# Kernel tuning notes

Measured on AMD Instinct MI355X. Metric: run time of the kernel, lower is better.

Reference implementation:

```python
import jax, jax.numpy as jnp
import numpy as np

SPATIAL_SHAPES = [(100, 100), (50, 50), (25, 25), (13, 13)]  # (h, w) per level
D_MODEL, N_HEADS, N_LEVELS, N_POINTS = 256, 8, 4, 4
B = 2
S = sum(h * w for h, w in SPATIAL_SHAPES)  # 13294
Q = S  # encoder self-attention: num_queries == sequence_length


def setup_inputs() -> dict:
    key = jax.random.key(0)
    ks = jax.random.split(key, 12)
    d = D_MODEL
    hlp = N_HEADS * N_LEVELS * N_POINTS
    scale = 0.02
    starts = np.cumsum([0] + [h * w for h, w in SPATIAL_SHAPES[:-1]])
    return {
        "hidden_states": jax.random.normal(ks[0], (B, Q, d), jnp.float32),
        "encoder_hidden_states": jax.random.normal(ks[1], (B, S, d), jnp.float32),
        "reference_points": jax.random.uniform(ks[2], (B, Q, N_LEVELS, 2), jnp.float32),
        "W_value": jax.random.normal(ks[3], (d, d), jnp.float32) * scale,
        "b_value": jnp.zeros((d,), jnp.float32),
        "W_off": jax.random.normal(ks[4], (d, hlp * 2), jnp.float32) * scale,
        "b_off": jax.random.normal(ks[5], (hlp * 2,), jnp.float32) * scale,
        "W_attn": jax.random.normal(ks[6], (d, hlp), jnp.float32) * scale,
        "b_attn": jnp.zeros((hlp,), jnp.float32),
        "W_out": jax.random.normal(ks[7], (d, d), jnp.float32) * scale,
        "b_out": jnp.zeros((d,), jnp.float32),
        "spatial_shapes": jnp.asarray(SPATIAL_SHAPES, jnp.int32),
        "level_start_index": jnp.asarray(starts, jnp.int32),
    }


def bilinear_sample(img, grid):
    # img: [N, C, h, w]; grid: [N, Q, P, 2] xy in [-1, 1]
    # F.grid_sample(mode='bilinear', padding_mode='zeros', align_corners=False)
    N, C, h, w = img.shape
    Qg, Pg = grid.shape[1], grid.shape[2]
    x = ((grid[..., 0] + 1.0) * w - 1.0) * 0.5
    y = ((grid[..., 1] + 1.0) * h - 1.0) * 0.5
    x0 = jnp.floor(x)
    y0 = jnp.floor(y)
    x1 = x0 + 1.0
    y1 = y0 + 1.0
    wx1 = x - x0
    wx0 = 1.0 - wx1
    wy1 = y - y0
    wy0 = 1.0 - wy1
    img_flat = img.reshape(N, C, h * w)

    def gather(xi, yi):
        valid = (xi >= 0) & (xi <= w - 1) & (yi >= 0) & (yi <= h - 1)
        xi_c = jnp.clip(xi, 0, w - 1).astype(jnp.int32)
        yi_c = jnp.clip(yi, 0, h - 1).astype(jnp.int32)
        idx = (yi_c * w + xi_c).reshape(N, 1, Qg * Pg)
        vals = jnp.take_along_axis(img_flat, idx, axis=2)  # [N, C, Q*P]
        return vals * valid.reshape(N, 1, Qg * Pg).astype(img.dtype)

    out = (
        gather(x0, y0) * (wx0 * wy0).reshape(N, 1, -1)
        + gather(x1, y0) * (wx1 * wy0).reshape(N, 1, -1)
        + gather(x0, y1) * (wx0 * wy1).reshape(N, 1, -1)
        + gather(x1, y1) * (wx1 * wy1).reshape(N, 1, -1)
    )
    return out.reshape(N, C, Qg, Pg)


def reference(hidden_states, encoder_hidden_states, reference_points,
              W_value, b_value, W_off, b_off, W_attn, b_attn, W_out, b_out,
              spatial_shapes, level_start_index):
    Bq, Qn, d = hidden_states.shape
    H, L, P = N_HEADS, N_LEVELS, N_POINTS
    Dh = d // H
    value = (encoder_hidden_states @ W_value + b_value).reshape(Bq, -1, H, Dh)
    off = (hidden_states @ W_off + b_off).reshape(Bq, Qn, H, L, P, 2)
    aw = (hidden_states @ W_attn + b_attn).reshape(Bq, Qn, H, L * P)
    aw = jax.nn.softmax(aw, axis=-1).reshape(Bq, Qn, H, L, P)
    # offset normalizer is (width, height) per level
    norm = jnp.stack([spatial_shapes[:, 1], spatial_shapes[:, 0]], -1).astype(off.dtype)
    loc = reference_points[:, :, None, :, None, :] + off / norm[None, None, None, :, None, :]
    grids = 2.0 * loc - 1.0  # [B, Q, H, L, P, 2]

    starts = np.cumsum([0] + [h * w for h, w in SPATIAL_SHAPES])
    sampled = []
    for lvl, (h, w) in enumerate(SPATIAL_SHAPES):
        v = value[:, starts[lvl]:starts[lvl + 1]]              # [B, h*w, H, Dh]
        v = v.transpose(0, 2, 3, 1).reshape(Bq * H, Dh, h, w)   # [B*H, Dh, h, w]
        g = grids[:, :, :, lvl].transpose(0, 2, 1, 3, 4).reshape(Bq * H, Qn, P, 2)
        sampled.append(bilinear_sample(v, g))                   # [B*H, Dh, Q, P]
    samp = jnp.stack(sampled, axis=-2).reshape(Bq * H, Dh, Qn, L * P)
    wts = aw.transpose(0, 2, 1, 3, 4).reshape(Bq * H, 1, Qn, L * P)
    out = (samp * wts).sum(-1)                                  # [B*H, Dh, Q]
    out = out.reshape(Bq, H * Dh, Qn).transpose(0, 2, 1)        # [B, Q, d]
    out = out @ W_out + b_out
    return out, aw
```

## Files before the change

kernel.cpp:

```cpp
#include <hip/hip_runtime.h>
#include <hip/hip_bf16.h>
#include <math.h>

#define BQn 2
#define QN 13294
#define SN 13294
#define NH 8
#define DH 32
#define DM 256

typedef __attribute__((ext_vector_type(8))) short short8;
typedef __attribute__((ext_vector_type(4))) float f32x4;

__device__ __forceinline__ unsigned short f2bf(float x) {
    union { float f; unsigned int u; } c; c.f = x;
    unsigned int r = c.u + 0x7fff + ((c.u >> 16) & 1);
    return (unsigned short)(r >> 16);
}
__device__ __forceinline__ float asf(unsigned int u) {
    union { unsigned int i; float f; } c; c.i = u; return c.f;
}

__global__ __launch_bounds__(256) void conv_weights(
    const float* __restrict__ Wv, const float* __restrict__ Woff,
    const float* __restrict__ Wa, const float* __restrict__ Wout,
    unsigned short* __restrict__ WvT, unsigned short* __restrict__ WoffT,
    unsigned short* __restrict__ WaT, unsigned short* __restrict__ WoutT)
{
    const int t = blockIdx.x * 256 + threadIdx.x;
    if (t < 65536) {
        const int n = t & 255, k = t >> 8;
        WvT[(size_t)n * 256 + k] = f2bf(Wv[(size_t)k * 256 + n]);
    } else if (t < 131072) {
        const int i = t - 65536, n = i & 255, k = i >> 8;
        WoffT[(size_t)n * 256 + k] = f2bf(Woff[(size_t)k * 256 + n]);
    } else if (t < 163840) {
        const int i = t - 131072, n = i & 127, k = i >> 7;
        WaT[(size_t)n * 256 + k] = f2bf(Wa[(size_t)k * 128 + n]);
    } else if (t < 229376) {
        const int i = t - 163840, n = i & 255, k = i >> 8;
        WoutT[(size_t)n * 256 + k] = f2bf(Wout[(size_t)k * 256 + n]);
    }
}

template<int N, int MODE, bool AF32>
__global__ __launch_bounds__(256) void gemm_mfma(
    const void* __restrict__ Av,
    const unsigned short* __restrict__ WT,
    const float* __restrict__ bias0,
    const float* __restrict__ bias1,
    void* __restrict__ Cv, int M)
{
    __shared__ unsigned short As[64][72];
    __shared__ unsigned short Bs[128][72];
    const int tid  = threadIdx.x;
    const int lane = tid & 63, wid = tid >> 6;
    const int wr = wid >> 1, wc = wid & 1;
    const int r0 = blockIdx.y * 64, n0 = blockIdx.x * 128;

    f32x4 acc[2][4] = {};

    for (int k0 = 0; k0 < 256; k0 += 64) {
        #pragma unroll
        for (int i = 0; i < 2; ++i) {
            const int idx = i * 256 + tid;
            const int row = idx >> 3, ch = (idx & 7) << 3;
            int grow = r0 + row; if (grow >= M) grow = M - 1;
            if (AF32) {
                const float* Af = (const float*)Av;
                const float4 v0 = *(const float4*)(Af + (size_t)grow * 256 + k0 + ch);
                const float4 v1 = *(const float4*)(Af + (size_t)grow * 256 + k0 + ch + 4);
                union { __hip_bfloat162 b[4]; uint4 u; } pk;
                pk.b[0] = __float22bfloat162_rn(make_float2(v0.x, v0.y));
                pk.b[1] = __float22bfloat162_rn(make_float2(v0.z, v0.w));
                pk.b[2] = __float22bfloat162_rn(make_float2(v1.x, v1.y));
                pk.b[3] = __float22bfloat162_rn(make_float2(v1.z, v1.w));
                *(uint4*)&As[row][ch] = pk.u;
            } else {
                const unsigned short* Ab = (const unsigned short*)Av;
                *(uint4*)&As[row][ch] =
                    *(const uint4*)(Ab + (size_t)grow * 256 + k0 + ch);
            }
        }
        #pragma unroll
        for (int i = 0; i < 4; ++i) {
            const int idx = i * 256 + tid;
            const int row = idx >> 3, ch = (idx & 7) << 3;
            *(uint4*)&Bs[row][ch] =
                *(const uint4*)(WT + (size_t)(n0 + row) * 256 + k0 + ch);
        }
        __syncthreads();
        #pragma unroll
        for (int kk = 0; kk < 2; ++kk) {
            const int kb = kk * 32 + (lane >> 4) * 8;
            short8 bfr[4];
            #pragma unroll
            for (int n = 0; n < 4; ++n)
                bfr[n] = *(const short8*)&Bs[wc * 64 + n * 16 + (lane & 15)][kb];
            #pragma unroll
            for (int m = 0; m < 2; ++m) {
                const short8 afr =
                    *(const short8*)&As[wr * 32 + m * 16 + (lane & 15)][kb];
                #pragma unroll
                for (int n = 0; n < 4; ++n)
                    acc[m][n] = __builtin_amdgcn_mfma_f32_16x16x32_bf16(
                        afr, bfr[n], acc[m][n], 0, 0, 0);
            }
        }
        __syncthreads();
    }

    #pragma unroll
    for (int m = 0; m < 2; ++m)
        #pragma unroll
        for (int n = 0; n < 4; ++n) {
            const int col = n0 + wc * 64 + n * 16 + (lane & 15);
            const float bsv = (col < 256) ? bias0[col] : bias1[col - 256];
            #pragma unroll
            for (int j = 0; j < 4; ++j) {
                const int row = r0 + wr * 32 + m * 16 + (lane >> 4) * 4 + j;
                if (row >= M) continue;
                const float v = acc[m][n][j] + bsv;
                if (MODE == 0) {
                    ((float*)Cv)[(size_t)row * N + col] = v;
                } else {
                    const int b = (row >= SN), s = row - b * SN;
                    const int h = col >> 5, dh = col & 31;
                    ((unsigned short*)Cv)
                        [(((size_t)b * NH + h) * SN + s) * DH + dh] = f2bf(v);
                }
            }
        }
}

__global__ __launch_bounds__(256) void ms_sample(
    const unsigned short* __restrict__ value,
    const float* __restrict__ offaw,
    const float* __restrict__ refp,
    unsigned short* __restrict__ outh,
    float* __restrict__ awout)
{
    const int h  = blockIdx.x & 7;
    const int qc = blockIdx.x >> 3;
    const int lc = threadIdx.x & 7;
    const int bq = qc * 32 + (threadIdx.x >> 3);
    if (bq >= BQn * QN) return;
    const int b  = (bq >= QN);
    const int gbase = threadIdx.x & 56;

    const float* rowp = offaw + (size_t)bq * 384;

    const float2 lw2 = *(const float2*)(rowp + 256 + h * 16 + lc * 2);
    float m = fmaxf(lw2.x, lw2.y);
    #pragma unroll
    for (int d = 1; d < 8; d <<= 1) m = fmaxf(m, __shfl_xor(m, d, 8));
    float e0 = __expf(lw2.x - m), e1 = __expf(lw2.y - m);
    float s = e0 + e1;
    #pragma unroll
    for (int d = 1; d < 8; d <<= 1) s += __shfl_xor(s, d, 8);
    const float inv = 1.f / s;
    e0 *= inv; e1 *= inv;
    *(float2*)(awout + (size_t)bq * 128 + h * 16 + lc * 2) = make_float2(e0, e1);

    const int lvl = lc >> 1;
    const int wi  = (lvl == 0) ? 100 : (lvl == 1) ? 50 : (lvl == 2) ? 25 : 13;
    const float fw = (float)wi;
    const int sti = (lvl == 0) ? 0 : (lvl == 1) ? 10000 : (lvl == 2) ? 12500 : 13125;
    const float rw = (lvl == 0) ? 0.01f : (lvl == 1) ? 0.02f
                   : (lvl == 2) ? 0.04f : (1.0f / 13.0f);
    const float2 rp = *(const float2*)(refp + (size_t)bq * 8 + lvl * 2);
    const float4 o4 = *(const float4*)(rowp + h * 32 + lc * 4);

    int   rA0, rB0, cA0, cB0, rA1, rB1, cA1, cB1;
    float wxA0, wxB0, wyA0, wyB0, wxA1, wxB1, wyA1, wyB1;

    auto prep = [&](float ox, float oy, float ek,
                    int& rA, int& rB, int& cA, int& cB,
                    float& wxA, float& wxB, float& wyA, float& wyB) {
        const float x = fmaf(fmaf(ox, rw, rp.x), fw, -0.5f);
        const float y = fmaf(fmaf(oy, rw, rp.y), fw, -0.5f);
        const float x0f = floorf(x), y0f = floorf(y);
        const int ix = (int)x0f, iy = (int)y0f;
        const float wx1 = x - x0f, wy1 = y - y0f;
        wxA = ((unsigned)ix        < (unsigned)wi) ? 1.f - wx1 : 0.f;
        wxB = ((unsigned)(ix + 1)  < (unsigned)wi) ? wx1       : 0.f;
        wyA = (((unsigned)iy       < (unsigned)wi) ? 1.f - wy1 : 0.f) * ek;
        wyB = (((unsigned)(iy + 1) < (unsigned)wi) ? wy1       : 0.f) * ek;
        const int xc0 = min(max(ix, 0),     wi - 1);
        const int xc1 = min(max(ix + 1, 0), wi - 1);
        const int yc0 = min(max(iy, 0),     wi - 1);
        const int yc1 = min(max(iy + 1, 0), wi - 1);
        rA = sti + yc0 * wi; rB = sti + yc1 * wi;
        cA = xc0;            cB = xc1;
    };
    prep(o4.x, o4.y, e0, rA0, rB0, cA0, cB0, wxA0, wxB0, wyA0, wyB0);
    prep(o4.z, o4.w, e1, rA1, rB1, cA1, cB1, wxA1, wxB1, wyA1, wyB1);

    const char* hplane = (const char*)(value + (size_t)h * SN * DH);
    const unsigned lnoff = (unsigned)b * (NH * SN * DH * 2) + lc * 8;

    float ax = 0.f, ay = 0.f, az = 0.f, aw_ = 0.f;

    #pragma unroll
    for (int p = 0; p < 16; ++p) {
        const int src = gbase + (p >> 1);
        const int   rA  = __shfl((p & 1) ? rA1  : rA0,  src, 64);
        const int   rB  = __shfl((p & 1) ? rB1  : rB0,  src, 64);
        const int   cA  = __shfl((p & 1) ? cA1  : cA0,  src, 64);
        const int   cB  = __shfl((p & 1) ? cB1  : cB0,  src, 64);
        const float wxA = __shfl((p & 1) ? wxA1 : wxA0, src, 64);
        const float wxB = __shfl((p & 1) ? wxB1 : wxB0, src, 64);
        const float wyA = __shfl((p & 1) ? wyA1 : wyA0, src, 64);
        const float wyB = __shfl((p & 1) ? wyB1 : wyB0, src, 64);

        #pragma unroll
        for (int c = 0; c < 4; ++c) {
            const int cell  = ((c >> 1) ? rB : rA) + ((c & 1) ? cB : cA);
            const float cw  = ((c & 1) ? wxB : wxA) * ((c >> 1) ? wyB : wyA);
            const uint2 v = *(const uint2*)(hplane + ((unsigned)cell * 64u + lnoff));
            ax  = fmaf(cw, asf(v.x << 16),          ax);
            ay  = fmaf(cw, asf(v.x & 0xffff0000u),  ay);
            az  = fmaf(cw, asf(v.y << 16),          az);
            aw_ = fmaf(cw, asf(v.y & 0xffff0000u),  aw_);
        }
    }

    ushort4 o;
    o.x = f2bf(ax); o.y = f2bf(ay); o.z = f2bf(az); o.w = f2bf(aw_);
    *(ushort4*)(outh + (size_t)bq * 256 + h * 32 + lc * 4) = o;
}

extern "C" void kernel_launch(void* const* d_in, const int* in_sizes, int n_in,
                              void* d_out, int out_size, void* d_ws, size_t ws_size,
                              hipStream_t stream) {
    const float* hs   = (const float*)d_in[0];
    const float* enc  = (const float*)d_in[1];
    const float* refp = (const float*)d_in[2];
    const float* Wv   = (const float*)d_in[3];
    const float* bv   = (const float*)d_in[4];
    const float* Woff = (const float*)d_in[5];
    const float* boff = (const float*)d_in[6];
    const float* Wa   = (const float*)d_in[7];
    const float* ba   = (const float*)d_in[8];
    const float* Wout = (const float*)d_in[9];
    const float* bout = (const float*)d_in[10];

    float* out    = (float*)d_out;
    float* aw_out = out + (size_t)BQn * QN * 256;

    const size_t MQ = (size_t)BQn * QN;
    unsigned short* valueb = (unsigned short*)d_ws;
    float* offaw = (float*)(valueb + MQ * 256);
    unsigned short* outh  = (unsigned short*)(offaw + MQ * 384);
    unsigned short* WvT   = outh + MQ * 256;
    unsigned short* WcatT = WvT + 256 * 256;
    unsigned short* WoutT = WcatT + 384 * 256;

    const int M = (int)MQ;
    const dim3 blk(256);

    conv_weights<<<896, blk, 0, stream>>>(Wv, Woff, Wa, Wout,
                                          WvT, WcatT, WcatT + 65536, WoutT);

    const int my = (M + 63) / 64;
    gemm_mfma<256, 1, true ><<<dim3(2, my), blk, 0, stream>>>(
        enc, WvT, bv, bv, valueb, M);
    gemm_mfma<384, 0, true ><<<dim3(3, my), blk, 0, stream>>>(
        hs, WcatT, boff, ba, offaw, M);

    const int qchunks = (M + 31) / 32;
    ms_sample<<<8 * qchunks, blk, 0, stream>>>(valueb, offaw, refp,
                                               outh, aw_out);

    gemm_mfma<256, 0, false><<<dim3(2, my), blk, 0, stream>>>(
        outh, WoutT, bout, bout, out, M);
}
```

Measured before the change: 130.2 us.

## Use 128-wide K tiles with register prefetch in the MFMA GEMM

The GEMM's K loop changes from four 64-wide tiles to two 128-wide tiles. Global loads for the second tile go into registers while MFMAs run on the first, which overlaps memory latency with compute and halves the number of barrier rounds. In exchange, shared memory roughly doubles and register pressure rises from the prefetch buffers, which may lower occupancy.

Result: slower. 181.8 us (+39.7%).

```diff
diff --git a/kernel.cpp b/kernel.cpp
--- a/kernel.cpp
+++ b/kernel.cpp
@@ -51,47 +51,70 @@
     const float* __restrict__ bias1,
     void* __restrict__ Cv, int M)
 {
-    __shared__ unsigned short As[64][72];
-    __shared__ unsigned short Bs[128][72];
+    __shared__ unsigned short As[64][136];
+    __shared__ unsigned short Bs[128][136];
     const int tid  = threadIdx.x;
     const int lane = tid & 63, wid = tid >> 6;
     const int wr = wid >> 1, wc = wid & 1;
     const int r0 = blockIdx.y * 64, n0 = blockIdx.x * 128;
 
-    f32x4 acc[2][4] = {};
-
-    for (int k0 = 0; k0 < 256; k0 += 64) {
-        #pragma unroll
-        for (int i = 0; i < 2; ++i) {
+    float4 paf[4][2];
+    uint4  pa[4];
+    uint4  pb[8];
+
+    auto LOADA = [&](int k0) {
+        #pragma unroll
+        for (int i = 0; i < 4; ++i) {
             const int idx = i * 256 + tid;
-            const int row = idx >> 3, ch = (idx & 7) << 3;
+            const int row = idx >> 4, ch = (idx & 15) << 3;
             int grow = r0 + row; if (grow >= M) grow = M - 1;
             if (AF32) {
                 const float* Af = (const float*)Av;
-                const float4 v0 = *(const float4*)(Af + (size_t)grow * 256 + k0 + ch);
-                const float4 v1 = *(const float4*)(Af + (size_t)grow * 256 + k0 + ch + 4);
+                paf[i][0] = *(const float4*)(Af + (size_t)grow * 256 + k0 + ch);
+                paf[i][1] = *(const float4*)(Af + (size_t)grow * 256 + k0 + ch + 4);
+            } else {
+                pa[i] = *(const uint4*)((const unsigned short*)Av
+                                        + (size_t)grow * 256 + k0 + ch);
+            }
+        }
+    };
+    auto LOADB = [&](int k0) {
+        #pragma unroll
+        for (int i = 0; i < 8; ++i) {
+            const int idx = i * 256 + tid;
+            const int row = idx >> 4, ch = (idx & 15) << 3;
+            pb[i] = *(const uint4*)(WT + (size_t)(n0 + row) * 256 + k0 + ch);
+        }
+    };
+    auto STORE = [&]() {
+        #pragma unroll
+        for (int i = 0; i < 4; ++i) {
+            const int idx = i * 256 + tid;
+            const int row = idx >> 4, ch = (idx & 15) << 3;
+            if (AF32) {
                 union { __hip_bfloat162 b[4]; uint4 u; } pk;
-                pk.b[0] = __float22bfloat162_rn(make_float2(v0.x, v0.y));
-                pk.b[1] = __float22bfloat162_rn(make_float2(v0.z, v0.w));
-                pk.b[2] = __float22bfloat162_rn(make_float2(v1.x, v1.y));
-                pk.b[3] = __float22bfloat162_rn(make_float2(v1.z, v1.w));
+                pk.b[0] = __float22bfloat162_rn(make_float2(paf[i][0].x, paf[i][0].y));
+                pk.b[1] = __float22bfloat162_rn(make_float2(paf[i][0].z, paf[i][0].w));
+                pk.b[2] = __float22bfloat162_rn(make_float2(paf[i][1].x, paf[i][1].y));
+                pk.b[3] = __float22bfloat162_rn(make_float2(paf[i][1].z, paf[i][1].w));
                 *(uint4*)&As[row][ch] = pk.u;
             } else {
-                const unsigned short* Ab = (const unsigned short*)Av;
-                *(uint4*)&As[row][ch] =
-                    *(const uint4*)(Ab + (size_t)grow * 256 + k0 + ch);
+                *(uint4*)&As[row][ch] = pa[i];
             }
         }
         #pragma unroll
-        for (int i = 0; i < 4; ++i) {
+        for (int i = 0; i < 8; ++i) {
             const int idx = i * 256 + tid;
-            const int row = idx >> 3, ch = (idx & 7) << 3;
-            *(uint4*)&Bs[row][ch] =
-                *(const uint4*)(WT + (size_t)(n0 + row) * 256 + k0 + ch);
-        }
-        __syncthreads();
-        #pragma unroll
-        for (int kk = 0; kk < 2; ++kk) {
+            const int row = idx >> 4, ch = (idx & 15) << 3;
+            *(uint4*)&Bs[row][ch] = pb[i];
+        }
+    };
+
+    f32x4 acc[2][4] = {};
+
+    auto MFMA_STEP = [&]() {
+        #pragma unroll
+        for (int kk = 0; kk < 4; ++kk) {
             const int kb = kk * 32 + (lane >> 4) * 8;
             short8 bfr[4];
             #pragma unroll
@@ -107,8 +130,17 @@
                         afr, bfr[n], acc[m][n], 0, 0, 0);
             }
         }
-        __syncthreads();
-    }
+    };
+
+    LOADA(0);  LOADB(0);
+    STORE();
+    __syncthreads();
+    LOADA(128); LOADB(128);
+    MFMA_STEP();
+    __syncthreads();
+    STORE();
+    __syncthreads();
+    MFMA_STEP();
 
     #pragma unroll
     for (int m = 0; m < 2; ++m)
```
